# Kernel tuning notes

Hardware: AMD Instinct MI355X
Metric: run time of the kernel (lower is better)

Reference implementation:

```python
import jax, jax.numpy as jnp
import numpy as np
from jax.scipy.linalg import solve_triangular

SIGMA2 = 1e-3   # Gaussian likelihood variance (fixed to 0.001 in the module)
JITTER = 1e-4   # settings.numerics.jitter_level (bumped for fp32)


def hankel(v, L):
    # Direct strided-gather formulation of the one-hot-matmul Hankel helper.
    # v: [N, D] -> [N-L+1, L*D]
    N, D = v.shape
    idx = jnp.arange(N - L + 1)[:, None] + jnp.arange(L)[None, :]  # [N-L+1, L]
    return v[idx].reshape(N - L + 1, L * D)


def setup_inputs() -> dict:
    key = jax.random.key(0)
    ks = jax.random.split(key, 5)
    N_data, Lt, Q, M, D = 2000, 10, 8, 256, 16
    N = N_data + Lt
    Din = Lt * Q
    Xm_m = jax.random.normal(ks[0], (N, Q), jnp.float32)
    Xm_v = jax.random.uniform(ks[1], (N, Q), jnp.float32, minval=0.01, maxval=0.5)
    Z = jax.random.normal(ks[2], (M, Din), jnp.float32)
    Y = jax.random.normal(ks[3], (N_data, D), jnp.float32)
    kern_var = jnp.float32(1.0)
    lengthscales = 8.0 + jax.random.uniform(ks[4], (Din,), jnp.float32)
    return {"Xm_m": Xm_m, "Xm_v": Xm_v, "Z": Z, "Y": Y,
            "kern_var": kern_var, "lengthscales": lengthscales, "Lt": Lt}


def reference(Xm_m, Xm_v, Z, Y, kern_var, lengthscales, Lt):
    dtype = Xm_m.dtype
    sigma2 = jnp.asarray(SIGMA2, dtype)
    sigma = jnp.sqrt(sigma2)

    # Hankel-embed means and variances of the latent sequence (drop first row).
    X_m = hankel(Xm_m[1:], Lt)  # [Nh, Din]
    X_v = hankel(Xm_v[1:], Lt)  # [Nh, Din]
    Nh = X_m.shape[0]           # == Y.shape[0] == N - Lt
    M = Z.shape[0]
    D = Y.shape[1]
    ls2 = lengthscales ** 2     # [Din]

    # Kuu: ARD RBF kernel on inducing points.
    zs = jnp.sum(Z ** 2 / ls2, axis=1)                              # [M]
    d2 = zs[:, None] + zs[None, :] - 2.0 * jnp.einsum('mq,nq->mn', Z / ls2, Z)  # [M,M]
    Kuu = kern_var * jnp.exp(-0.5 * d2) + JITTER * jnp.eye(M, dtype=dtype)

    # psi0 = sum_n eKdiag = Nh * sigma_f^2
    psi0 = Nh * kern_var

    # psi1[n,m] = sf2 * prod_q (Xv/ls2+1)^-1/2 * exp(-0.5 (mu-z)^2/(Xv+ls2))
    d1 = X_v + ls2                                                   # [Nh,Din]
    e1 = (jnp.sum(X_m ** 2 / d1, axis=1)[:, None]
          - 2.0 * jnp.einsum('nq,mq->nm', X_m / d1, Z)
          + jnp.einsum('nq,mq->nm', 1.0 / d1, Z ** 2))               # [Nh,M]
    logc1 = -0.5 * jnp.sum(jnp.log1p(X_v / ls2), axis=1)             # [Nh]
    psi1 = kern_var * jnp.exp(-0.5 * e1 + logc1[:, None])            # [Nh,M]

    # psi2 = sum_n sf4 * exp(-(zm-zm')^2/(4ls2)) * prod_q (2Xv/ls2+1)^-1/2
    #        * exp(-(mu - zbar)^2/(2Xv+ls2))
    zbar = 0.5 * (Z[:, None, :] + Z[None, :, :])                     # [M,M,Din]
    distfac = jnp.exp(-0.25 * d2)                                    # [M,M]
    d2v = 2.0 * X_v + ls2                                            # [Nh,Din]
    e2 = (jnp.sum(X_m ** 2 / d2v, axis=1)[:, None, None]
          - 2.0 * jnp.einsum('nq,abq->nab', X_m / d2v, zbar)
          + jnp.einsum('nq,abq->nab', 1.0 / d2v, zbar ** 2))         # [Nh,M,M]
    logc2 = -0.5 * jnp.sum(jnp.log1p(2.0 * X_v / ls2), axis=1)       # [Nh]
    psi2 = (kern_var ** 2) * distfac * jnp.sum(jnp.exp(-e2 + logc2[:, None, None]), axis=0)  # [M,M]

    # Sparse-variational GP lower bound (Titsias/GPLVM style).
    L = jnp.linalg.cholesky(Kuu)
    A = solve_triangular(L, psi1.T, lower=True) / sigma              # [M,Nh]
    tmp = solve_triangular(L, psi2, lower=True)
    AAT = solve_triangular(L, tmp.T, lower=True) / sigma2            # [M,M]
    B = AAT + jnp.eye(M, dtype=dtype)
    LB = jnp.linalg.cholesky(B)
    log_det_B = 2.0 * jnp.sum(jnp.log(jnp.diag(LB)))
    c = solve_triangular(LB, A @ Y, lower=True) / sigma              # [M,D]

    bound = -0.5 * Nh * D * jnp.log(2.0 * jnp.pi * sigma2)
    bound = bound - 0.5 / sigma2 * jnp.sum(Y ** 2)
    bound = bound - 0.5 * D * (psi0 / sigma2 - jnp.trace(AAT))
    bound = bound - 0.5 * D * log_det_B
    bound = bound + 0.5 * jnp.sum(c ** 2)
    return bound
```

## Files before the change

kernel.cpp:

```cpp
#include <hip/hip_runtime.h>
#include <math.h>

#define NH   2000
#define QD   8
#define DIN  80
#define MI   256
#define DOUT 16
#define SIGMA2     1e-3f
#define INV_SIGMA2 1000.0f
#define JITTER     1e-4f



__global__ void k_prep(const float* __restrict__ Xm_v, const float* __restrict__ Y,
                       const float* __restrict__ ls, float* __restrict__ vbar,
                       float* __restrict__ acc) {
    __shared__ float red[256];
    int tid = threadIdx.x;
    int b = blockIdx.x;
    if (b < DIN) {
        int j = b;
        int l = j >> 3, qq = j & 7;
        float lsv = ls[j];
        float ls2 = lsv * lsv;
        float s = 0.f;
        for (int n = tid; n < NH; n += 256) {
            float xv = Xm_v[(1 + n + l) * QD + qq];
            s += 1.0f / (2.0f * xv + ls2);
        }
        red[tid] = s;
        __syncthreads();
        for (int st = 128; st > 0; st >>= 1) {
            if (tid < st) red[tid] += red[tid + st];
            __syncthreads();
        }
        if (tid == 0) vbar[j] = red[0] * (1.0f / NH);
    } else {
        const float4* y4 = (const float4*)Y;
        float sy = 0.f;
        for (int i = (b - DIN) * 256 + tid; i < NH * DOUT / 4; i += 8 * 256) {
            float4 y = y4[i];
            sy += y.x * y.x + y.y * y.y + y.z * y.z + y.w * y.w;
        }
        red[tid] = sy;
        __syncthreads();
        for (int st = 128; st > 0; st >>= 1) {
            if (tid < st) red[tid] += red[tid + st];
            __syncthreads();
        }
        if (tid == 0) acc[b - DIN] = red[0];
    }
}

__global__ void k_main(const float* __restrict__ Xm_m, const float* __restrict__ Xm_v,
                       const float* __restrict__ Z, const float* __restrict__ ls,
                       const float* __restrict__ kvp,
                       float* __restrict__ psi1, float* __restrict__ Eg) {
    __shared__ __align__(16) float xm[DIN], h1[DIN], v2[DIN];
    __shared__ float red1[DIN], red2[DIN];
    __shared__ float sc[2];
    int tid = threadIdx.x;
    int n = blockIdx.x;
    if (tid < DIN) {
        int j = tid;
        int l = j >> 3, qq = j & 7;
        int row = 1 + n + l;
        float xmv = Xm_m[row * QD + qq];
        float xvv = Xm_v[row * QD + qq];
        float lsv = ls[j];
        float ls2 = lsv * lsv;
        float iv1 = 1.0f / (xvv + ls2);
        float iv2 = 1.0f / (2.0f * xvv + ls2);
        xm[j] = xmv; h1[j] = 0.5f * iv1; v2[j] = iv2;
        red1[j] = 0.5f * __logf(ls2 * iv1);
        red2[j] = 0.25f * __logf(ls2 * iv2) - 0.5f * xmv * xmv * iv2;
    }
    __syncthreads();
    if (tid == 0) {
        float a = 0.f, b = 0.f;
        for (int j = 0; j < DIN; ++j) { a += red1[j]; b += red2[j]; }
        sc[0] = a; sc[1] = b;
    }
    __syncthreads();
    float c1 = sc[0], c2h = sc[1];
    const float4* zr  = (const float4*)(Z + tid * DIN);
    const float4* xm4 = (const float4*)xm;
    const float4* h14 = (const float4*)h1;
    const float4* v24 = (const float4*)v2;
    float e1h = 0.f, P = 0.f;
    #pragma unroll 4
    for (int j4 = 0; j4 < DIN / 4; ++j4) {
        float4 z = zr[j4], x = xm4[j4], h = h14[j4], v = v24[j4];
        float d;
        d = z.x - x.x; e1h += h.x * d * d; P += v.x * z.x * (0.25f * z.x - x.x);
        d = z.y - x.y; e1h += h.y * d * d; P += v.y * z.y * (0.25f * z.y - x.y);
        d = z.z - x.z; e1h += h.z * d * d; P += v.z * z.z * (0.25f * z.z - x.z);
        d = z.w - x.w; e1h += h.w * d * d; P += v.w * z.w * (0.25f * z.w - x.w);
    }
    float kv = kvp[0];
    psi1[n * MI + tid] = kv * __expf(c1 - e1h);
    Eg [n * MI + tid] = __expf(c2h - P);
}

__global__ void k_kuuF(const float* __restrict__ Z, const float* __restrict__ ls,
                       const float* __restrict__ vbar, const float* __restrict__ kvp,
                       float* __restrict__ Kuu, float* __restrict__ F) {
    __shared__ __align__(16) float ils2[DIN];
    int tid = threadIdx.x;
    int b = blockIdx.x;
    if (tid < DIN) { float l = ls[tid]; ils2[tid] = 1.0f / (l * l); }
    __syncthreads();
    const float4* za4 = (const float4*)(Z + tid * DIN);
    const float4* zb4 = (const float4*)(Z + b * DIN);
    const float4* il4 = (const float4*)ils2;
    const float4* vb4 = (const float4*)vbar;
    float d2a = 0.f, c0 = 0.f;
    #pragma unroll 4
    for (int j4 = 0; j4 < DIN / 4; ++j4) {
        float4 za = za4[j4], zb = zb4[j4], il = il4[j4], vb = vb4[j4];
        float d;
        d = za.x - zb.x; d2a += d * d * il.x; c0 += vb.x * za.x * zb.x;
        d = za.y - zb.y; d2a += d * d * il.y; c0 += vb.y * za.y * zb.y;
        d = za.z - zb.z; d2a += d * d * il.z; c0 += vb.z * za.z * zb.z;
        d = za.w - zb.w; d2a += d * d * il.w; c0 += vb.w * za.w * zb.w;
    }
    float kv = kvp[0];
    int a = tid;
    Kuu[b * MI + a] = kv * __expf(-0.5f * d2a) + (a == b ? JITTER : 0.f);
    F  [b * MI + a] = kv * kv * __expf(-0.25f * d2a - 0.5f * c0);
}

__global__ void k_syrk(const float* __restrict__ Eg, float* __restrict__ Spart,
                       int rowsPer) {
    __shared__ __align__(16) float As[16 * 64], Bs[16 * 64];
    int tid = threadIdx.x;
    int ta = blockIdx.x & 3, tb = blockIdx.x >> 2;
    int k0 = blockIdx.y * rowsPer;
    int tx = tid & 15, ty = tid >> 4;
    float acc[4][4] = {};
    for (int kk = k0; kk < k0 + rowsPer; kk += 16) {
        __syncthreads();
        for (int i = tid; i < 1024; i += 256) {
            int k = i >> 6, c = i & 63;
            As[k * 64 + c] = Eg[(kk + k) * MI + 64 * ta + c];
            Bs[k * 64 + c] = Eg[(kk + k) * MI + 64 * tb + c];
        }
        __syncthreads();
        #pragma unroll
        for (int k = 0; k < 16; ++k) {
            float4 a4 = *(const float4*)&As[k * 64 + 4 * tx];
            float4 b4 = *(const float4*)&Bs[k * 64 + 4 * ty];
            float a[4] = {a4.x, a4.y, a4.z, a4.w};
            float b[4] = {b4.x, b4.y, b4.z, b4.w};
            #pragma unroll
            for (int i = 0; i < 4; ++i)
                #pragma unroll
                for (int j = 0; j < 4; ++j)
                    acc[i][j] += a[i] * b[j];
        }
    }
    float* out = Spart + blockIdx.y * (MI * MI);
    #pragma unroll
    for (int i = 0; i < 4; ++i)
        #pragma unroll
        for (int j = 0; j < 4; ++j)
            out[(64 * ta + 4 * tx + i) * MI + 64 * tb + 4 * ty + j] = acc[i][j];
}

__global__ void k_psi2M(const float* __restrict__ F, const float* __restrict__ Spart,
                        const float* __restrict__ Kuu,
                        float* __restrict__ S, float* __restrict__ M2, int nsplit) {
    int i = blockIdx.x * 256 + threadIdx.x;
    float s = 0.f;
    for (int y = 0; y < nsplit; ++y) s += Spart[y * (MI * MI) + i];
    float v = F[i] * s;
    S[i] = v;
    M2[i] = Kuu[i] + INV_SIGMA2 * v;
}

__global__ void k_G(const float* __restrict__ psi1, const float* __restrict__ Y,
                    float* __restrict__ Gpart) {
    __shared__ float Ys[25 * DOUT];
    int a = threadIdx.x;
    int n0 = blockIdx.x * 25;
    for (int i = a; i < 25 * DOUT; i += 256) Ys[i] = Y[n0 * DOUT + i];
    __syncthreads();
    float acc[DOUT] = {};
    #pragma unroll
    for (int m = 0; m < 25; ++m) {
        float p = psi1[(n0 + m) * MI + a];
        #pragma unroll
        for (int d = 0; d < DOUT; ++d) acc[d] += p * Ys[m * DOUT + d];
    }
    float4* out = (float4*)(Gpart + blockIdx.x * (MI * DOUT) + a * DOUT);
    out[0] = make_float4(acc[0], acc[1], acc[2], acc[3]);
    out[1] = make_float4(acc[4], acc[5], acc[6], acc[7]);
    out[2] = make_float4(acc[8], acc[9], acc[10], acc[11]);
    out[3] = make_float4(acc[12], acc[13], acc[14], acc[15]);
}

__global__ void k_Gsum(const float* __restrict__ Gpart, float* __restrict__ G) {
    int gid = blockIdx.x * 256 + threadIdx.x;
    float s = 0.f;
    for (int b = 0; b < 80; ++b) s += Gpart[b * (MI * DOUT) + gid];
    G[gid] = s;
}

__global__ void k_dchol(float* __restrict__ AK, float* __restrict__ AM,
                        float* __restrict__ LiK, float* __restrict__ LiM,
                        float* __restrict__ acc, int p) {
    float* A  = blockIdx.x ? AM : AK;
    float* Li = blockIdx.x ? LiM : LiK;
    const int c0 = 64 * p;
    __shared__ float colA[2][64], colB[2][64];
    __shared__ float rowEA[2][64], rowEB[2][64];
    __shared__ float isr[64];
    int tid = threadIdx.x;
    int tx = tid & 15;
    int ty = tid >> 4;
    bool isA = ty < 16;
    int cb = isA ? 4 * ty : 4 * (ty - 16);
    float t[4][4];
    if (isA) {
        #pragma unroll
        for (int i = 0; i < 4; ++i)
            #pragma unroll
            for (int j = 0; j < 4; ++j)
                t[i][j] = A[(c0 + 4 * tx + i) * MI + c0 + cb + j];
    } else {
        #pragma unroll
        for (int i = 0; i < 4; ++i)
            #pragma unroll
            for (int j = 0; j < 4; ++j)
                t[i][j] = (4 * tx + i == cb + j) ? 1.f : 0.f;
    }
    if (isA && ty == 0) {
        #pragma unroll
        for (int i = 0; i < 4; ++i) {
            colA[0][4 * tx + i] = t[i][0];
            colB[0][4 * tx + i] = t[i][1];
        }
    }
    if (tid < 64) {
        rowEA[0][tid] = (tid == 0) ? 1.f : 0.f;
        rowEB[0][tid] = (tid == 1) ? 1.f : 0.f;
    }
    __syncthreads();
    float lgsum = 0.f;
    for (int s = 0; s < 32; ++s) {
        int pb = s & 1;
        int k0 = 2 * s, k1 = 2 * s + 1;
        float pk0 = colA[pb][k0];
        float ip0 = 1.0f / pk0;
        float m10 = colA[pb][k1] * ip0;
        float pk1 = colB[pb][k1] - m10 * colA[pb][k1];
        float ip1 = 1.0f / pk1;
        if (tid == 0) {
            isr[k0] = rsqrtf(pk0); isr[k1] = rsqrtf(pk1);
            lgsum += __logf(pk0) + __logf(pk1);
        }
        float a0[4], a1[4], b0[4], b1[4];
        #pragma unroll
        for (int i = 0; i < 4; ++i) {
            int r = 4 * tx + i;
            float cA = colA[pb][r], cB = colB[pb][r];
            a0[i] = (r > k0) ? cA * ip0 : 0.f;
            a1[i] = (r > k1) ? (cB - m10 * cA) * ip1 : 0.f;
        }
        if (isA) {
            #pragma unroll
            for (int j = 0; j < 4; ++j) {
                int c = cb + j;
                float cA = colA[pb][c], cB = colB[pb][c];
                b0[j] = (c > k0) ? cA : 0.f;
                b1[j] = (c > k1) ? (cB - m10 * cA) : 0.f;
            }
        } else {
            #pragma unroll
            for (int j = 0; j < 4; ++j) {
                float eA = rowEA[pb][cb + j], eB = rowEB[pb][cb + j];
                b0[j] = eA;
                b1[j] = eB - m10 * eA;
            }
        }
        #pragma unroll
        for (int i = 0; i < 4; ++i)
            #pragma unroll
            for (int j = 0; j < 4; ++j) {
                t[i][j] = fmaf(-a0[i], b0[j], t[i][j]);
                t[i][j] = fmaf(-a1[i], b1[j], t[i][j]);
            }
        if (s < 31) {
            int kn0 = k0 + 2, kn1 = k0 + 3;
            if (isA && ty == (kn0 >> 2)) {
                int j0 = kn0 & 3;
                #pragma unroll
                for (int jj = 0; jj < 4; ++jj) {
                    if (jj == j0) {
                        #pragma unroll
                        for (int i = 0; i < 4; ++i) colA[1 - pb][4 * tx + i] = t[i][jj];
                    }
                    if (jj == j0 + 1) {
                        #pragma unroll
                        for (int i = 0; i < 4; ++i) colB[1 - pb][4 * tx + i] = t[i][jj];
                    }
                }
            }
            if (!isA && tx == (kn0 >> 2)) {
                int i0 = kn0 & 3;
                #pragma unroll
                for (int ii = 0; ii < 4; ++ii) {
                    if (ii == i0) {
                        #pragma unroll
                        for (int j = 0; j < 4; ++j) rowEA[1 - pb][cb + j] = t[ii][j];
                    }
                    if (ii == i0 + 1) {
                        #pragma unroll
                        for (int j = 0; j < 4; ++j) rowEB[1 - pb][cb + j] = t[ii][j];
                    }
                }
            }
        }
        __syncthreads();
    }
    if (tid == 0) acc[8 + 4 * blockIdx.x + p] = lgsum;
    if (!isA) {
        #pragma unroll
        for (int i = 0; i < 4; ++i) {
            int r = 4 * tx + i;
            float sc = isr[r];
            #pragma unroll
            for (int j = 0; j < 4; ++j)
                Li[(c0 + r) * MI + c0 + cb + j] = t[i][j] * sc;
        }
    }
    for (int jb = p + 1; jb < 4; ++jb)
        for (int q = tid; q < 4096; q += 512) {
            int rr = q >> 6, cc = q & 63;
            Li[(c0 + rr) * MI + 64 * jb + cc] = 0.f;
        }
}

__global__ void k_trsm(float* __restrict__ AK, float* __restrict__ AM,
                       const float* __restrict__ LiK, const float* __restrict__ LiM,
                       int p) {
    float* A = blockIdx.y ? AM : AK;
    const float* Li = blockIdx.y ? LiM : LiK;
    int c0 = 64 * p;
    int R0 = c0 + 64 + 64 * blockIdx.x;
    __shared__ float As[64 * 68], Bs[64 * 68];
    int tid = threadIdx.x;
    int tx = tid & 15, ty = tid >> 4;
    for (int q = tid; q < 4096; q += 256) {
        int rr = q >> 6, k = q & 63;
        As[k * 68 + rr] = A[(R0 + rr) * MI + c0 + k];
        Bs[k * 68 + rr] = Li[(c0 + rr) * MI + c0 + k];
    }
    __syncthreads();
    float acc[4][4] = {};
    #pragma unroll 4
    for (int k = 0; k < 64; ++k) {
        float4 a4 = *(const float4*)&As[k * 68 + 4 * tx];
        float4 b4 = *(const float4*)&Bs[k * 68 + 4 * ty];
        float a[4] = {a4.x, a4.y, a4.z, a4.w};
        float b[4] = {b4.x, b4.y, b4.z, b4.w};
        #pragma unroll
        for (int i = 0; i < 4; ++i)
            #pragma unroll
            for (int j = 0; j < 4; ++j)
                acc[i][j] += a[i] * b[j];
    }
    #pragma unroll
    for (int i = 0; i < 4; ++i)
        #pragma unroll
        for (int j = 0; j < 4; ++j)
            A[(R0 + 4 * tx + i) * MI + c0 + 4 * ty + j] = acc[i][j];
}

__global__ void k_cholu(float* __restrict__ AK, float* __restrict__ AM, int p) {
    float* A = blockIdx.y ? AM : AK;
    int t0 = 64 * (p + 1);
    int idx = blockIdx.x, ti = 0;
    while (idx > ti) { idx -= ti + 1; ti++; }
    int tj = idx;
    int R0 = t0 + 64 * ti, C0 = t0 + 64 * tj, K0 = 64 * p;
    __shared__ float As[64 * 68], Bs[64 * 68];
    int tid = threadIdx.x;
    int tx = tid & 15, ty = tid >> 4;
    for (int q = tid; q < 4096; q += 256) {
        int rr = q >> 6, k = q & 63;
        As[k * 68 + rr] = A[(R0 + rr) * MI + K0 + k];
        Bs[k * 68 + rr] = A[(C0 + rr) * MI + K0 + k];
    }
    __syncthreads();
    float acc[4][4] = {};
    #pragma unroll 4
    for (int k = 0; k < 64; ++k) {
        float4 a4 = *(const float4*)&As[k * 68 + 4 * tx];
        float4 b4 = *(const float4*)&Bs[k * 68 + 4 * ty];
        float a[4] = {a4.x, a4.y, a4.z, a4.w};
        float b[4] = {b4.x, b4.y, b4.z, b4.w};
        #pragma unroll
        for (int i = 0; i < 4; ++i)
            #pragma unroll
            for (int j = 0; j < 4; ++j)
                acc[i][j] += a[i] * b[j];
    }
    #pragma unroll
    for (int i = 0; i < 4; ++i)
        #pragma unroll
        for (int j = 0; j < 4; ++j) {
            int g = (R0 + 4 * tx + i) * MI + C0 + 4 * ty + j;
            A[g] -= acc[i][j];
        }
}

__global__ void k_toff(const float* __restrict__ LAK, const float* __restrict__ LAM,
                       float* __restrict__ LiK, float* __restrict__ LiM, int d) {
    const float* LA = blockIdx.y ? LAM : LAK;
    float* Li = blockIdx.y ? LiM : LiK;
    int j = blockIdx.x, i = j + d;
    __shared__ float As[64 * 68], Bs[64 * 68];
    int tid = threadIdx.x;
    int tx = tid & 15, ty = tid >> 4;
    float acc[4][4] = {};
    for (int m = 0; m < d; ++m) {
        int kb = j + m;
        __syncthreads();
        for (int q = tid; q < 4096; q += 256) {
            int rr = q >> 6, k = q & 63;
            As[k * 68 + rr] = LA[(64 * i + rr) * MI + 64 * kb + k];
        }
        for (int q = tid; q < 4096; q += 256) {
            int k = q >> 6, c = q & 63;
            Bs[k * 68 + c] = Li[(64 * kb + k) * MI + 64 * j + c];
        }
        __syncthreads();
        #pragma unroll 4
        for (int k = 0; k < 64; ++k) {
            float4 a4 = *(const float4*)&As[k * 68 + 4 * tx];
            float4 b4 = *(const float4*)&Bs[k * 68 + 4 * ty];
            float a[4] = {a4.x, a4.y, a4.z, a4.w};
            float b[4] = {b4.x, b4.y, b4.z, b4.w};
            #pragma unroll
            for (int i2 = 0; i2 < 4; ++i2)
                #pragma unroll
                for (int j2 = 0; j2 < 4; ++j2)
                    acc[i2][j2] += a[i2] * b[j2];
        }
    }
    __syncthreads();
    #pragma unroll
    for (int i2 = 0; i2 < 4; ++i2)
        #pragma unroll
        for (int j2 = 0; j2 < 4; ++j2)
            Bs[(4 * tx + i2) * 68 + 4 * ty + j2] = acc[i2][j2];
    for (int q = tid; q < 4096; q += 256) {
        int rr = q >> 6, k = q & 63;
        As[k * 68 + rr] = Li[(64 * i + rr) * MI + 64 * i + k];
    }
    __syncthreads();
    float out[4][4] = {};
    #pragma unroll 4
    for (int k = 0; k < 64; ++k) {
        float4 a4 = *(const float4*)&As[k * 68 + 4 * tx];
        float4 b4 = *(const float4*)&Bs[k * 68 + 4 * ty];
        float a[4] = {a4.x, a4.y, a4.z, a4.w};
        float b[4] = {b4.x, b4.y, b4.z, b4.w};
        #pragma unroll
        for (int i2 = 0; i2 < 4; ++i2)
            #pragma unroll
            for (int j2 = 0; j2 < 4; ++j2)
                out[i2][j2] += a[i2] * b[j2];
    }
    #pragma unroll
    for (int i2 = 0; i2 < 4; ++i2)
        #pragma unroll
        for (int j2 = 0; j2 < 4; ++j2)
            Li[(64 * i + 4 * tx + i2) * MI + 64 * j + 4 * ty + j2] = -out[i2][j2];
}

__global__ void k_trace(const float* __restrict__ Li, const float* __restrict__ S,
                        float* __restrict__ Tpart) {
    int R = 64 * (blockIdx.x >> 2), C = 64 * (blockIdx.x & 3);
    int k0 = 16 * blockIdx.y;
    int slot = blockIdx.y * 16 + blockIdx.x;
    if (C > R || k0 >= R + 64) {
        if (threadIdx.x == 0) Tpart[slot] = 0.f;
        return;
    }
    __shared__ __align__(16) float As[16 * 68], Bs[16 * 68];
    __shared__ float red[256];
    int tid = threadIdx.x;
    int tx = tid & 15, ty = tid >> 4;
    for (int q = tid; q < 1024; q += 256) {
        int rr = q >> 4, kk = q & 15;
        As[kk * 68 + rr] = Li[(R + rr) * MI + k0 + kk];
    }
    for (int q = tid; q < 1024; q += 256) {
        int kk = q >> 6, c = q & 63;
        Bs[kk * 68 + c] = S[(k0 + kk) * MI + C + c];
    }
    __syncthreads();
    float acc4[4][4] = {};
    #pragma unroll
    for (int k = 0; k < 16; ++k) {
        float4 a4 = *(const float4*)&As[k * 68 + 4 * tx];
        float4 b4 = *(const float4*)&Bs[k * 68 + 4 * ty];
        float a[4] = {a4.x, a4.y, a4.z, a4.w};
        float b[4] = {b4.x, b4.y, b4.z, b4.w};
        #pragma unroll
        for (int i = 0; i < 4; ++i)
            #pragma unroll
            for (int j = 0; j < 4; ++j)
                acc4[i][j] += a[i] * b[j];
    }
    float ts = 0.f;
    #pragma unroll
    for (int i = 0; i < 4; ++i)
        #pragma unroll
        for (int j = 0; j < 4; ++j)
            ts += acc4[i][j] * Li[(R + 4 * tx + i) * MI + C + 4 * ty + j];
    red[tid] = ts;
    __syncthreads();
    for (int st = 128; st > 0; st >>= 1) {
        if (tid < st) red[tid] += red[tid + st];
        __syncthreads();
    }
    if (tid == 0) Tpart[slot] = red[0];
}

__global__ void k_final(const float* __restrict__ LiM, const float* __restrict__ G,
                        const float* __restrict__ Tpart,
                        const float* __restrict__ accbuf, const float* __restrict__ kvp,
                        float* __restrict__ out) {
    __shared__ float Gs[MI * DOUT];
    __shared__ float red[256], redT[256];
    __shared__ float accs[16];
    int tid = threadIdx.x;
    for (int i = tid; i < MI * DOUT; i += 256) Gs[i] = G[i];
    redT[tid] = Tpart[tid];
    if (tid < 16) accs[tid] = accbuf[tid];
    __syncthreads();
    float w[DOUT] = {};
    const float4* lrow4 = (const float4*)(LiM + tid * MI);
    for (int k4 = 0; k4 < MI / 4; ++k4) {
        float4 l = lrow4[k4];
        const float* g0 = &Gs[(4 * k4) * DOUT];
        #pragma unroll
        for (int d = 0; d < DOUT; ++d)
            w[d] += l.x * g0[d] + l.y * g0[DOUT + d] + l.z * g0[2 * DOUT + d] + l.w * g0[3 * DOUT + d];
    }
    float c2 = 0.f;
    #pragma unroll
    for (int d = 0; d < DOUT; ++d) c2 += w[d] * w[d];
    red[tid] = c2;
    __syncthreads();
    for (int st = 128; st > 0; st >>= 1) {
        if (tid < st) { red[tid] += red[tid + st]; redT[tid] += redT[tid + st]; }
        __syncthreads();
    }
    if (tid == 0) {
        float kv = kvp[0];
        float sumY2 = 0.f, ldK = 0.f, ldM = 0.f;
        for (int i = 0; i < 8; ++i) sumY2 += accs[i];
        for (int i = 8; i < 12; ++i) ldK += accs[i];
        for (int i = 12; i < 16; ++i) ldM += accs[i];
        float trace = redT[0] * INV_SIGMA2;
        float logdetB = ldM - ldK;
        float bound = -0.5f * (float)(NH * DOUT) * __logf(6.28318530717959f * SIGMA2)
                      - 0.5f * INV_SIGMA2 * sumY2
                      - 0.5f * (float)DOUT * ((float)NH * kv * INV_SIGMA2 - trace)
                      - 0.5f * (float)DOUT * logdetB
                      + 0.5f * 1.0e6f * red[0];
        out[0] = bound;
    }
}

extern "C" void kernel_launch(void* const* d_in, const int* in_sizes, int n_in,
                              void* d_out, int out_size, void* d_ws, size_t ws_size,
                              hipStream_t stream) {
    (void)in_sizes; (void)n_in; (void)out_size;
    const float* Xm_m = (const float*)d_in[0];
    const float* Xm_v = (const float*)d_in[1];
    const float* Z    = (const float*)d_in[2];
    const float* Y    = (const float*)d_in[3];
    const float* kvp  = (const float*)d_in[4];
    const float* ls   = (const float*)d_in[5];
    float* out = (float*)d_out;
    float* W = (float*)d_ws;

    float* acc   = W;
    float* Tpart = W + 16;
    float* G     = W + 272;
    float* LinvK = W + 4368;
    float* LinvM = W + 69904;
    float* vbar  = W + 135440;
    float* psi1  = W + 135520;
    float* Eg    = W + 647520;
    float* Kuu   = W + 1159520;
    float* M2    = W + 1225056;
    float* S     = W + 1290592;
    float* F     = W + 1356128;
    float* Spart = W + 1421664;

    int nsplit = (ws_size >= (size_t)(1421664 + 25 * 65536 + 80 * 4096) * 4) ? 25 : 5;
    int rowsPer = NH / nsplit;
    float* Gpart = Spart + (size_t)nsplit * 65536;

    k_prep<<<DIN + 8, 256, 0, stream>>>(Xm_v, Y, ls, vbar, acc);
    k_main<<<NH, 256, 0, stream>>>(Xm_m, Xm_v, Z, ls, kvp, psi1, Eg);
    k_kuuF<<<MI, 256, 0, stream>>>(Z, ls, vbar, kvp, Kuu, F);
    k_syrk<<<dim3(16, nsplit), 256, 0, stream>>>(Eg, Spart, rowsPer);
    k_psi2M<<<MI, 256, 0, stream>>>(F, Spart, Kuu, S, M2, nsplit);
    k_G<<<80, 256, 0, stream>>>(psi1, Y, Gpart);
    k_Gsum<<<16, 256, 0, stream>>>(Gpart, G);

    for (int p = 0; p < 4; ++p) {
        k_dchol<<<2, 512, 0, stream>>>(Kuu, M2, LinvK, LinvM, acc, p);
        if (p < 3) {
            k_trsm<<<dim3(3 - p, 2), 256, 0, stream>>>(Kuu, M2, LinvK, LinvM, p);
            int nt = 3 - p;
            k_cholu<<<dim3(nt * (nt + 1) / 2, 2), 256, 0, stream>>>(Kuu, M2, p);
        }
    }
    for (int d = 1; d < 4; ++d)
        k_toff<<<dim3(4 - d, 2), 256, 0, stream>>>(Kuu, M2, LinvK, LinvM, d);

    k_trace<<<dim3(16, 16), 256, 0, stream>>>(LinvK, S, Tpart);
    k_final<<<1, 256, 0, stream>>>(LinvM, G, Tpart, acc, kvp, out);
}
```

Before: 353.5 us.

## Transpose Z for coalesced loads and fuse TRSM panel into diagonal Cholesky kernel

```diff
diff --git a/kernel.cpp b/kernel.cpp
--- a/kernel.cpp
+++ b/kernel.cpp
@@ -11,6 +11,12 @@
 #define JITTER     1e-4f
 
 
+
+__global__ void k_zt(const float* __restrict__ Z, float* __restrict__ Zt) {
+    int j = blockIdx.x;
+    int m = threadIdx.x;
+    Zt[j * MI + m] = Z[m * DIN + j];
+}
 
 __global__ void k_prep(const float* __restrict__ Xm_v, const float* __restrict__ Y,
                        const float* __restrict__ ls, float* __restrict__ vbar,
@@ -53,10 +59,10 @@
 }
 
 __global__ void k_main(const float* __restrict__ Xm_m, const float* __restrict__ Xm_v,
-                       const float* __restrict__ Z, const float* __restrict__ ls,
+                       const float* __restrict__ Zt, const float* __restrict__ ls,
                        const float* __restrict__ kvp,
                        float* __restrict__ psi1, float* __restrict__ Eg) {
-    __shared__ __align__(16) float xm[DIN], h1[DIN], v2[DIN];
+    __shared__ float xm[DIN], h1[DIN], v2[DIN];
     __shared__ float red1[DIN], red2[DIN];
     __shared__ float sc[2];
     int tid = threadIdx.x;
@@ -83,46 +89,41 @@
     }
     __syncthreads();
     float c1 = sc[0], c2h = sc[1];
-    const float4* zr  = (const float4*)(Z + tid * DIN);
-    const float4* xm4 = (const float4*)xm;
-    const float4* h14 = (const float4*)h1;
-    const float4* v24 = (const float4*)v2;
     float e1h = 0.f, P = 0.f;
-    #pragma unroll 4
-    for (int j4 = 0; j4 < DIN / 4; ++j4) {
-        float4 z = zr[j4], x = xm4[j4], h = h14[j4], v = v24[j4];
-        float d;
-        d = z.x - x.x; e1h += h.x * d * d; P += v.x * z.x * (0.25f * z.x - x.x);
-        d = z.y - x.y; e1h += h.y * d * d; P += v.y * z.y * (0.25f * z.y - x.y);
-        d = z.z - x.z; e1h += h.z * d * d; P += v.z * z.z * (0.25f * z.z - x.z);
-        d = z.w - x.w; e1h += h.w * d * d; P += v.w * z.w * (0.25f * z.w - x.w);
+    #pragma unroll 8
+    for (int j = 0; j < DIN; ++j) {
+        float z = Zt[j * MI + tid];
+        float d = z - xm[j];
+        e1h += h1[j] * d * d;
+        P += v2[j] * z * (0.25f * z - xm[j]);
     }
     float kv = kvp[0];
     psi1[n * MI + tid] = kv * __expf(c1 - e1h);
     Eg [n * MI + tid] = __expf(c2h - P);
 }
 
-__global__ void k_kuuF(const float* __restrict__ Z, const float* __restrict__ ls,
+__global__ void k_kuuF(const float* __restrict__ Zt, const float* __restrict__ Z,
+                       const float* __restrict__ ls,
                        const float* __restrict__ vbar, const float* __restrict__ kvp,
                        float* __restrict__ Kuu, float* __restrict__ F) {
-    __shared__ __align__(16) float ils2[DIN];
+    __shared__ float ils2[DIN], zbs[DIN], vb[DIN];
     int tid = threadIdx.x;
     int b = blockIdx.x;
-    if (tid < DIN) { float l = ls[tid]; ils2[tid] = 1.0f / (l * l); }
-    __syncthreads();
-    const float4* za4 = (const float4*)(Z + tid * DIN);
-    const float4* zb4 = (const float4*)(Z + b * DIN);
-    const float4* il4 = (const float4*)ils2;
-    const float4* vb4 = (const float4*)vbar;
+    if (tid < DIN) {
+        float l = ls[tid];
+        ils2[tid] = 1.0f / (l * l);
+        zbs[tid] = Z[b * DIN + tid];
+        vb[tid] = vbar[tid];
+    }
+    __syncthreads();
     float d2a = 0.f, c0 = 0.f;
-    #pragma unroll 4
-    for (int j4 = 0; j4 < DIN / 4; ++j4) {
-        float4 za = za4[j4], zb = zb4[j4], il = il4[j4], vb = vb4[j4];
-        float d;
-        d = za.x - zb.x; d2a += d * d * il.x; c0 += vb.x * za.x * zb.x;
-        d = za.y - zb.y; d2a += d * d * il.y; c0 += vb.y * za.y * zb.y;
-        d = za.z - zb.z; d2a += d * d * il.z; c0 += vb.z * za.z * zb.z;
-        d = za.w - zb.w; d2a += d * d * il.w; c0 += vb.w * za.w * zb.w;
+    #pragma unroll 8
+    for (int j = 0; j < DIN; ++j) {
+        float za = Zt[j * MI + tid];
+        float zb = zbs[j];
+        float d = za - zb;
+        d2a += d * d * ils2[j];
+        c0 += vb[j] * za * zb;
     }
     float kv = kvp[0];
     int a = tid;
@@ -215,6 +216,8 @@
     __shared__ float colA[2][64], colB[2][64];
     __shared__ float rowEA[2][64], rowEB[2][64];
     __shared__ float isr[64];
+    __shared__ float LsT[64 * 64];
+    __shared__ float As[64 * 64];
     int tid = threadIdx.x;
     int tx = tid & 15;
     int ty = tid >> 4;
@@ -291,7 +294,7 @@
                 t[i][j] = fmaf(-a1[i], b1[j], t[i][j]);
             }
         if (s < 31) {
-            int kn0 = k0 + 2, kn1 = k0 + 3;
+            int kn0 = k0 + 2;
             if (isA && ty == (kn0 >> 2)) {
                 int j0 = kn0 & 3;
                 #pragma unroll
@@ -330,8 +333,11 @@
             int r = 4 * tx + i;
             float sc = isr[r];
             #pragma unroll
-            for (int j = 0; j < 4; ++j)
-                Li[(c0 + r) * MI + c0 + cb + j] = t[i][j] * sc;
+            for (int j = 0; j < 4; ++j) {
+                float v = t[i][j] * sc;
+                Li[(c0 + r) * MI + c0 + cb + j] = v;
+                LsT[(cb + j) * 64 + r] = v;
+            }
         }
     }
     for (int jb = p + 1; jb < 4; ++jb)
@@ -339,42 +345,39 @@
             int rr = q >> 6, cc = q & 63;
             Li[(c0 + rr) * MI + 64 * jb + cc] = 0.f;
         }
-}
-
-__global__ void k_trsm(float* __restrict__ AK, float* __restrict__ AM,
-                       const float* __restrict__ LiK, const float* __restrict__ LiM,
-                       int p) {
-    float* A = blockIdx.y ? AM : AK;
-    const float* Li = blockIdx.y ? LiM : LiK;
-    int c0 = 64 * p;
-    int R0 = c0 + 64 + 64 * blockIdx.x;
-    __shared__ float As[64 * 68], Bs[64 * 68];
-    int tid = threadIdx.x;
-    int tx = tid & 15, ty = tid >> 4;
-    for (int q = tid; q < 4096; q += 256) {
-        int rr = q >> 6, k = q & 63;
-        As[k * 68 + rr] = A[(R0 + rr) * MI + c0 + k];
-        Bs[k * 68 + rr] = Li[(c0 + rr) * MI + c0 + k];
-    }
-    __syncthreads();
-    float acc[4][4] = {};
-    #pragma unroll 4
-    for (int k = 0; k < 64; ++k) {
-        float4 a4 = *(const float4*)&As[k * 68 + 4 * tx];
-        float4 b4 = *(const float4*)&Bs[k * 68 + 4 * ty];
-        float a[4] = {a4.x, a4.y, a4.z, a4.w};
-        float b[4] = {b4.x, b4.y, b4.z, b4.w};
-        #pragma unroll
-        for (int i = 0; i < 4; ++i)
-            #pragma unroll
-            for (int j = 0; j < 4; ++j)
-                acc[i][j] += a[i] * b[j];
-    }
-    #pragma unroll
-    for (int i = 0; i < 4; ++i)
-        #pragma unroll
-        for (int j = 0; j < 4; ++j)
-            A[(R0 + 4 * tx + i) * MI + c0 + 4 * ty + j] = acc[i][j];
+    if (p < 3) {
+        __syncthreads();
+        for (int rb = 0; rb < 3 - p; ++rb) {
+            int R0 = c0 + 64 + 64 * rb;
+            for (int q = tid; q < 4096; q += 512) {
+                int rr = q >> 6, k = q & 63;
+                As[k * 64 + rr] = A[(R0 + rr) * MI + c0 + k];
+            }
+            __syncthreads();
+            if (tid < 256) {
+                int txc = tid & 15, tyc = tid >> 4;
+                float acc4[4][4] = {};
+                #pragma unroll 4
+                for (int k = 0; k < 64; ++k) {
+                    float4 a4 = *(const float4*)&As[k * 64 + 4 * txc];
+                    float4 b4 = *(const float4*)&LsT[k * 64 + 4 * tyc];
+                    float a[4] = {a4.x, a4.y, a4.z, a4.w};
+                    float b[4] = {b4.x, b4.y, b4.z, b4.w};
+                    #pragma unroll
+                    for (int i = 0; i < 4; ++i)
+                        #pragma unroll
+                        for (int j = 0; j < 4; ++j)
+                            acc4[i][j] += a[i] * b[j];
+                }
+                #pragma unroll
+                for (int i = 0; i < 4; ++i)
+                    #pragma unroll
+                    for (int j = 0; j < 4; ++j)
+                        A[(R0 + 4 * txc + i) * MI + c0 + 4 * tyc + j] = acc4[i][j];
+            }
+            __syncthreads();
+        }
+    }
 }
 
 __global__ void k_cholu(float* __restrict__ AK, float* __restrict__ AM, int p) {
@@ -602,15 +605,17 @@
     float* M2    = W + 1225056;
     float* S     = W + 1290592;
     float* F     = W + 1356128;
-    float* Spart = W + 1421664;
-
-    int nsplit = (ws_size >= (size_t)(1421664 + 25 * 65536 + 80 * 4096) * 4) ? 25 : 5;
+    float* Zt    = W + 1421664;
+    float* Spart = W + 1442144;
+
+    int nsplit = (ws_size >= (size_t)(1442144 + 25 * 65536 + 80 * 4096) * 4) ? 25 : 5;
     int rowsPer = NH / nsplit;
     float* Gpart = Spart + (size_t)nsplit * 65536;
 
+    k_zt<<<DIN, 256, 0, stream>>>(Z, Zt);
     k_prep<<<DIN + 8, 256, 0, stream>>>(Xm_v, Y, ls, vbar, acc);
-    k_main<<<NH, 256, 0, stream>>>(Xm_m, Xm_v, Z, ls, kvp, psi1, Eg);
-    k_kuuF<<<MI, 256, 0, stream>>>(Z, ls, vbar, kvp, Kuu, F);
+    k_main<<<NH, 256, 0, stream>>>(Xm_m, Xm_v, Zt, ls, kvp, psi1, Eg);
+    k_kuuF<<<MI, 256, 0, stream>>>(Zt, Z, ls, vbar, kvp, Kuu, F);
     k_syrk<<<dim3(16, nsplit), 256, 0, stream>>>(Eg, Spart, rowsPer);
     k_psi2M<<<MI, 256, 0, stream>>>(F, Spart, Kuu, S, M2, nsplit);
     k_G<<<80, 256, 0, stream>>>(psi1, Y, Gpart);
@@ -619,7 +624,6 @@
     for (int p = 0; p < 4; ++p) {
         k_dchol<<<2, 512, 0, stream>>>(Kuu, M2, LinvK, LinvM, acc, p);
         if (p < 3) {
-            k_trsm<<<dim3(3 - p, 2), 256, 0, stream>>>(Kuu, M2, LinvK, LinvM, p);
             int nt = 3 - p;
             k_cholu<<<dim3(nt * (nt + 1) / 2, 2), 256, 0, stream>>>(Kuu, M2, p);
         }
```

After: 356.2 us. About the same (+0.8%).
